# Kernel tuning notes

Hardware: AMD Instinct MI355X
Metric: run time of the kernel (lower is better)

Reference implementation:

```python
import jax, jax.numpy as jnp
import numpy as np

B, N, E, H = 16, 196, 512, 8   # batch, tokens(14x14), embedding_channels(=KV_size_S), heads
HD = E // H                    # 64  spatial-attn head dim
C = 4 * E                      # 2048 = KV_size (concat of 4 branches)
HDC = C // H                   # 256 channel-attn (SelfAttentionTAT) head dim

def _ln(x, g, b, eps=1e-6):
    m = jnp.mean(x, -1, keepdims=True)
    v = jnp.mean(jnp.square(x - m), -1, keepdims=True)
    return (x - m) * jax.lax.rsqrt(v + eps) * g + b

def setup_inputs():
    key = jax.random.key(0)
    ks = jax.random.split(key, 16)
    n = lambda k, s, sc=0.02: jax.random.normal(k, s, jnp.float32) * sc
    return {
        "emb1": jax.random.normal(ks[0], (B, N, E), jnp.float32),
        "emb2": jax.random.normal(ks[1], (B, N, E), jnp.float32),
        "emb3": jax.random.normal(ks[2], (B, N, E), jnp.float32),
        "emb4": jax.random.normal(ks[3], (B, N, E), jnp.float32),
        "ln_attn_g": jnp.ones((4, E), jnp.float32), "ln_attn_b": jnp.zeros((4, E), jnp.float32),
        "lnC_g": jnp.ones((C,), jnp.float32), "lnC_b": jnp.zeros((C,), jnp.float32),
        "Wq_c": n(ks[4], (C, C)), "Wk_c": n(ks[5], (C, C)),
        "Wv_c": n(ks[6], (C, C)), "Wo_c": n(ks[7], (C, C)),
        "q_w": n(ks[8], (4, N, N), 0.05),              # query1..4 stacked (token-mixing Linear(196,196))
        "k_w": n(ks[9], (4 * N, 4 * N)),               # key   Linear(784,784)
        "v_w": n(ks[10], (4 * N, 4 * N)),              # value Linear(784,784)
        "out_w": n(ks[11], (4, E, E)),                 # out1..4 stacked
        "ln_ffn_g": jnp.ones((4, E), jnp.float32), "ln_ffn_b": jnp.zeros((4, E), jnp.float32),
        "fc1_w": n(ks[12], (4, E, 4 * E)), "fc1_b": n(ks[13], (4, 4 * E), 1e-6),
        "fc2_w": n(ks[14], (4, 4 * E, E)), "fc2_b": n(ks[15], (4, E), 1e-6),
    }

def reference(emb1, emb2, emb3, emb4, ln_attn_g, ln_attn_b, lnC_g, lnC_b,
              Wq_c, Wk_c, Wv_c, Wo_c, q_w, k_w, v_w, out_w,
              ln_ffn_g, ln_ffn_b, fc1_w, fc1_b, fc2_w, fc2_b):
    embs = jnp.stack([emb1, emb2, emb3, emb4])                         # [4,B,N,E]
    cx = _ln(embs, ln_attn_g[:, None, None, :], ln_attn_b[:, None, None, :])
    ec = _ln(jnp.concatenate([emb1, emb2, emb3, emb4], -1), lnC_g, lnC_b)  # [B,N,C]
    # SelfAttentionTAT: multi-head self-attention over the concatenated channel embedding
    q = (ec @ Wq_c).reshape(B, N, H, HDC).transpose(0, 2, 1, 3)
    k = (ec @ Wk_c).reshape(B, N, H, HDC).transpose(0, 2, 1, 3)
    v = (ec @ Wv_c).reshape(B, N, H, HDC).transpose(0, 2, 1, 3)
    s = jax.nn.softmax(jnp.einsum('bhnd,bhmd->bhnm', q, k) * np.float32(1.0 / np.sqrt(HDC)), -1)
    T_hat = jnp.einsum('bhnm,bhmd->bhnd', s, v).transpose(0, 2, 1, 3).reshape(B, N, C) @ Wo_c
    # split channel dim into 4 chunks, concat along token axis -> [B,4N,E]
    KV_S = T_hat.reshape(B, N, 4, E).transpose(0, 2, 1, 3).reshape(B, 4 * N, E)
    # token-mixing projections (Linear applied to the token axis)
    Q = jnp.einsum('gbnc,gnm->gbmc', cx, q_w)                          # [4,B,N,E]
    K = jnp.einsum('bnc,nm->bmc', KV_S, k_w)                           # [B,4N,E]
    V = jnp.einsum('bnc,nm->bmc', KV_S, v_w)
    Qh = Q.reshape(4, B, N, H, HD).transpose(0, 1, 3, 2, 4)            # [4,B,H,N,HD]
    Kh = K.reshape(B, 4 * N, H, HD).transpose(0, 2, 1, 3)              # [B,H,4N,HD]
    Vh = V.reshape(B, 4 * N, H, HD).transpose(0, 2, 1, 3)
    attn = jnp.einsum('gbhnd,bhmd->gbhnm', Qh, Kh)                     # [4,B,H,N,4N]
    # InstanceNorm2d (no affine, eps=1e-5) over (N,4N) per (branch,batch,head) instead of 1/sqrt(d)
    m = jnp.mean(attn, (-2, -1), keepdims=True)
    var = jnp.mean(jnp.square(attn - m), (-2, -1), keepdims=True)
    p = jax.nn.softmax((attn - m) * jax.lax.rsqrt(var + 1e-5), -1)
    ctx = jnp.einsum('gbhnm,bhmd->gbhnd', p, Vh)                       # [4,B,H,N,HD]
    # faithful to source: only branch 1 is permuted before .view; branches 2-4
    # are .view'ed directly from [B,H,N,HD] (head-major flatten)
    c1 = ctx[0].transpose(0, 2, 1, 3).reshape(B, N, E)
    crest = ctx[1:].reshape(3, B, N, E)
    cmerged = jnp.concatenate([c1[None], crest], 0)                    # [4,B,N,E]
    h = embs + jnp.einsum('gbne,gef->gbnf', cmerged, out_w)            # residual 1
    x = _ln(h, ln_ffn_g[:, None, None, :], ln_ffn_b[:, None, None, :])
    x = jax.nn.gelu(jnp.einsum('gbne,gef->gbnf', x, fc1_w) + fc1_b[:, None, None, :], approximate=False)
    x = jnp.einsum('gbnf,gfe->gbne', x, fc2_w) + fc2_b[:, None, None, :]
    out = x + h                                                        # residual 2
    return (out[0], out[1], out[2], out[3])
```

## Files before the change

### kernel.cpp

```cpp
#include <hip/hip_runtime.h>
#include <hip/hip_bf16.h>
#include <math.h>

typedef __hip_bfloat16 bf16;
typedef __attribute__((ext_vector_type(8))) short v8s;
typedef __attribute__((ext_vector_type(4))) short v4s;
typedef __attribute__((ext_vector_type(4))) float v4f;

#define Bq   16
#define Nq   196
#define Eq   512
#define Hq   8
#define HDq  64
#define Cq   2048
#define HDCq 256
#define N4q  784
#define BNq  (Bq*Nq)
#define SLOT ((long)BNq*Cq)
#define L2E  1.44269504f

struct P4 { const void* p[4]; };

__global__ __launch_bounds__(256) void k_fill(float* __restrict__ out, long n, float v) {
  long i = (long)blockIdx.x * 256 + threadIdx.x;
  if (i < n) out[i] = v;
}

__device__ __forceinline__ float blk_sum(float v, float* buf) {
  #pragma unroll
  for (int off = 32; off; off >>= 1) v += __shfl_down(v, off, 64);
  int tid = threadIdx.x;
  __syncthreads();
  if ((tid & 63) == 0) buf[tid >> 6] = v;
  __syncthreads();
  return buf[0] + buf[1] + buf[2] + buf[3];
}

__device__ __forceinline__ unsigned int pack2bf(float a, float b) {
  unsigned short ha = __builtin_bit_cast(unsigned short, (bf16)a);
  unsigned short hb = __builtin_bit_cast(unsigned short, (bf16)b);
  return (unsigned int)ha | ((unsigned int)hb << 16);
}

__global__ __launch_bounds__(256) void k_ln_concat(
    const float* __restrict__ e1, const float* __restrict__ e2,
    const float* __restrict__ e3, const float* __restrict__ e4,
    const float* __restrict__ gamma, const float* __restrict__ beta,
    bf16* __restrict__ ec) {
  __shared__ float buf[4];
  int row = blockIdx.x;
  int tid = threadIdx.x;
  float vals[8];
  #pragma unroll
  for (int i = 0; i < 8; i++) {
    const float* src = (i < 2) ? e1 : (i < 4) ? e2 : (i < 6) ? e3 : e4;
    vals[i] = src[(long)row * Eq + (i & 1) * 256 + tid];
  }
  float s = 0;
  #pragma unroll
  for (int i = 0; i < 8; i++) s += vals[i];
  float mean = blk_sum(s, buf) * (1.f / 2048.f);
  float ss = 0;
  #pragma unroll
  for (int i = 0; i < 8; i++) { float d = vals[i] - mean; ss += d * d; }
  float rstd = rsqrtf(blk_sum(ss, buf) * (1.f / 2048.f) + 1e-6f);
  #pragma unroll
  for (int i = 0; i < 8; i++) {
    int c = tid + i * 256;
    ec[(long)row * Cq + c] = (bf16)((vals[i] - mean) * rstd * gamma[c] + beta[c]);
  }
}

__global__ __launch_bounds__(256) void k_ln_branch(
    const float* __restrict__ e1, const float* __restrict__ e2,
    const float* __restrict__ e3, const float* __restrict__ e4,
    const float* __restrict__ gamma, const float* __restrict__ beta,
    bf16* __restrict__ cx) {
  __shared__ float buf[4];
  int idx = blockIdx.x;
  int tid = threadIdx.x;
  int row = idx % BNq; int g = idx / BNq;
  const float* src = (g == 0) ? e1 : (g == 1) ? e2 : (g == 2) ? e3 : e4;
  float v0 = src[(long)row * Eq + tid];
  float v1 = src[(long)row * Eq + 256 + tid];
  float mean = blk_sum(v0 + v1, buf) * (1.f / 512.f);
  float d0 = v0 - mean, d1 = v1 - mean;
  float var = blk_sum(d0 * d0 + d1 * d1, buf) * (1.f / 512.f);
  float rstd = rsqrtf(var + 1e-6f);
  cx[(long)idx * Eq + tid]       = (bf16)(d0 * rstd * gamma[g * Eq + tid]       + beta[g * Eq + tid]);
  cx[(long)idx * Eq + 256 + tid] = (bf16)(d1 * rstd * gamma[g * Eq + 256 + tid] + beta[g * Eq + 256 + tid]);
}

__global__ __launch_bounds__(256) void k_ln_rows(
    const bf16* __restrict__ x, const float* __restrict__ gamma, const float* __restrict__ beta,
    bf16* __restrict__ out) {
  __shared__ float buf[4];
  int idx = blockIdx.x;
  int tid = threadIdx.x;
  int g = idx / BNq;
  float v0 = (float)x[(long)idx * Eq + tid];
  float v1 = (float)x[(long)idx * Eq + 256 + tid];
  float mean = blk_sum(v0 + v1, buf) * (1.f / 512.f);
  float d0 = v0 - mean, d1 = v1 - mean;
  float var = blk_sum(d0 * d0 + d1 * d1, buf) * (1.f / 512.f);
  float rstd = rsqrtf(var + 1e-6f);
  out[(long)idx * Eq + tid]       = (bf16)(d0 * rstd * gamma[g * Eq + tid]       + beta[g * Eq + tid]);
  out[(long)idx * Eq + 256 + tid] = (bf16)(d1 * rstd * gamma[g * Eq + 256 + tid] + beta[g * Eq + 256 + tid]);
}

__global__ __launch_bounds__(256) void k_cvt_t(
    const float* __restrict__ W, bf16* __restrict__ WT, int K, int Nn) {
  __shared__ short T[64][72];
  int tid = threadIdx.x;
  long zo = (long)blockIdx.z * K * Nn;
  int n0 = blockIdx.x * 64, k0 = blockIdx.y * 64;
  int r = tid >> 2, c = (tid & 3) * 16;
  const float* src = W + zo + (long)(k0 + r) * Nn + n0 + c;
  float4 f0 = *(const float4*)src;
  float4 f1 = *(const float4*)(src + 4);
  float4 f2 = *(const float4*)(src + 8);
  float4 f3 = *(const float4*)(src + 12);
  float fv[16] = {f0.x,f0.y,f0.z,f0.w, f1.x,f1.y,f1.z,f1.w,
                  f2.x,f2.y,f2.z,f2.w, f3.x,f3.y,f3.z,f3.w};
  #pragma unroll
  for (int e = 0; e < 16; e++)
    T[c + e][r] = __builtin_bit_cast(short, (bf16)fv[e]);
  __syncthreads();
  short* dst = (short*)WT + zo + (long)(n0 + r) * K + k0 + c;
  *(v8s*)dst       = *(const v8s*)&T[r][c];
  *(v8s*)(dst + 8) = *(const v8s*)&T[r][c + 8];
}

template<bool HAS_BIAS, bool GELU, int RES_MODE, bool OUT_F32>
__global__ __launch_bounds__(256, 2) void k_gemm_bt(
    const bf16* __restrict__ A, const bf16* __restrict__ WT,
    const float* __restrict__ bias, P4 resp,
    void* __restrict__ out, int M, int Nn, int K,
    long aStride, long wStride, long oStride) {
  __shared__ short As[256][76];
  __shared__ short Bs[64][76];
  int tid = threadIdx.x;
  int l = tid & 63, w = tid >> 6;
  int li = l & 15, lg = l >> 4;
  int z = blockIdx.z;
  int m0 = blockIdx.x * 256, n0 = blockIdx.y * 64;
  const short* Ab = (const short*)A + (long)z * aStride;
  const short* Wb = (const short*)WT + (long)z * wStride;
  const void* res = resp.p[z];

  v4f acc[4][4] = {};

  int ar = tid >> 1, ak = (tid & 1) * 32;
  long arow0 = (long)m0 + ar;       if (arow0 >= M) arow0 = M - 1;
  long arow1 = (long)m0 + ar + 128; if (arow1 >= M) arow1 = M - 1;
  const short* ap0 = Ab + arow0 * K + ak;
  const short* ap1 = Ab + arow1 * K + ak;
  int br = tid >> 2, bk = (tid & 3) * 16;
  const short* bp = Wb + (long)(n0 + br) * K + bk;

  for (int k0 = 0; k0 < K; k0 += 64) {
    const short* p0 = ap0 + k0;
    const short* p1 = ap1 + k0;
    *(v8s*)&As[ar][ak]            = *(const v8s*)p0;
    *(v8s*)&As[ar][ak + 8]        = *(const v8s*)(p0 + 8);
    *(v8s*)&As[ar][ak + 16]       = *(const v8s*)(p0 + 16);
    *(v8s*)&As[ar][ak + 24]       = *(const v8s*)(p0 + 24);
    *(v8s*)&As[ar + 128][ak]      = *(const v8s*)p1;
    *(v8s*)&As[ar + 128][ak + 8]  = *(const v8s*)(p1 + 8);
    *(v8s*)&As[ar + 128][ak + 16] = *(const v8s*)(p1 + 16);
    *(v8s*)&As[ar + 128][ak + 24] = *(const v8s*)(p1 + 24);
    *(v8s*)&Bs[br][bk]            = *(const v8s*)(bp + k0);
    *(v8s*)&Bs[br][bk + 8]        = *(const v8s*)(bp + k0 + 8);
    __syncthreads();
    #pragma unroll
    for (int ks = 0; ks < 2; ks++) {
      v8s af[4], bfr[4];
      #pragma unroll
      for (int mi = 0; mi < 4; mi++)
        af[mi] = *(const v8s*)&As[w * 64 + mi * 16 + li][ks * 32 + lg * 8];
      #pragma unroll
      for (int nj = 0; nj < 4; nj++)
        bfr[nj] = *(const v8s*)&Bs[nj * 16 + li][ks * 32 + lg * 8];
      #pragma unroll
      for (int mi = 0; mi < 4; mi++)
        #pragma unroll
        for (int nj = 0; nj < 4; nj++)
          acc[mi][nj] = __builtin_amdgcn_mfma_f32_16x16x32_bf16(af[mi], bfr[nj], acc[mi][nj], 0, 0, 0);
    }
    __syncthreads();
  }

  #pragma unroll
  for (int nj = 0; nj < 4; nj++) {
    int n = n0 + nj * 16 + li;
    float bv = HAS_BIAS ? bias[n] : 0.f;
    #pragma unroll
    for (int mi = 0; mi < 4; mi++) {
      #pragma unroll
      for (int rr = 0; rr < 4; rr++) {
        int m = m0 + w * 64 + mi * 16 + lg * 4 + rr;
        if (m < M) {
          float x = acc[mi][nj][rr] + bv;
          if (GELU) x = 0.5f * x * (1.f + erff(x * 0.70710678118f));
          if (RES_MODE == 1) x += ((const float*)res)[(long)m * Nn + n];
          if (RES_MODE == 2) x += (float)((const bf16*)res)[(long)m * Nn + n];
          if (OUT_F32) (((float*)out) + (long)z * oStride)[(long)m * Nn + n] = x;
          else         (((bf16*)out)  + (long)z * oStride)[(long)m * Nn + n] = (bf16)x;
        }
      }
    }
  }
}

template<bool HAS_BIAS, bool GELU, int RES_MODE, bool OUT_F32>
__global__ __launch_bounds__(256, 2) void k_gemm(
    const bf16* __restrict__ A, const float* __restrict__ W,
    const float* __restrict__ bias, const void* __restrict__ res,
    void* __restrict__ out, int M, int Nn, int K,
    long aStride, long wStride, long bStride, long resStride, long oStride) {
  __shared__ short As[256][76];
  __shared__ short Bs[64][72];
  int tid = threadIdx.x;
  int l = tid & 63, w = tid >> 6;
  int li = l & 15, lg = l >> 4;
  int z = blockIdx.z;
  int m0 = blockIdx.x * 256, n0 = blockIdx.y * 64;
  const short* Ab = (const short*)A + (long)z * aStride;
  const float* Wb = W + (long)z * wStride;
  const float* biasb = HAS_BIAS ? bias + (long)z * bStride : nullptr;
  const float* resF = (RES_MODE == 1) ? (const float*)res + (long)z * resStride : nullptr;
  const bf16*  resB = (RES_MODE == 2) ? (const bf16*)res + (long)z * resStride : nullptr;

  v4f acc[4][4] = {};

  int ar = tid >> 1, ak = (tid & 1) * 32;
  long arow0 = (long)m0 + ar;       if (arow0 >= M) arow0 = M - 1;
  long arow1 = (long)m0 + ar + 128; if (arow1 >= M) arow1 = M - 1;
  const short* ap0 = Ab + arow0 * K + ak;
  const short* ap1 = Ab + arow1 * K + ak;

  for (int k0 = 0; k0 < K; k0 += 64) {
    {
      const short* p0 = ap0 + k0;
      const short* p1 = ap1 + k0;
      *(v8s*)&As[ar][ak]            = *(const v8s*)p0;
      *(v8s*)&As[ar][ak + 8]        = *(const v8s*)(p0 + 8);
      *(v8s*)&As[ar][ak + 16]       = *(const v8s*)(p0 + 16);
      *(v8s*)&As[ar][ak + 24]       = *(const v8s*)(p0 + 24);
      *(v8s*)&As[ar + 128][ak]      = *(const v8s*)p1;
      *(v8s*)&As[ar + 128][ak + 8]  = *(const v8s*)(p1 + 8);
      *(v8s*)&As[ar + 128][ak + 16] = *(const v8s*)(p1 + 16);
      *(v8s*)&As[ar + 128][ak + 24] = *(const v8s*)(p1 + 24);
    }
    #pragma unroll
    for (int t = 0; t < 2; t++) {
      int p = tid + 256 * t;
      int kp = p >> 4, nf = p & 15;
      const float* wp = Wb + (long)(k0 + 2 * kp) * Nn + n0 + nf * 4;
      float4 w0 = *(const float4*)wp;
      float4 w1 = *(const float4*)(wp + Nn);
      float f0[4] = {w0.x, w0.y, w0.z, w0.w};
      float f1[4] = {w1.x, w1.y, w1.z, w1.w};
      int ko = (2 * kp) ^ ((nf & 7) << 3);
      #pragma unroll
      for (int e = 0; e < 4; e++)
        *(unsigned int*)&Bs[nf * 4 + e][ko] = pack2bf(f0[e], f1[e]);
    }
    __syncthreads();
    #pragma unroll
    for (int ks = 0; ks < 2; ks++) {
      v8s af[4], bfr[4];
      #pragma unroll
      for (int mi = 0; mi < 4; mi++)
        af[mi] = *(const v8s*)&As[w * 64 + mi * 16 + li][ks * 32 + lg * 8];
      #pragma unroll
      for (int nj = 0; nj < 4; nj++) {
        int rn = nj * 16 + li;
        int ko = (ks * 32 + lg * 8) ^ (((rn >> 2) & 7) << 3);
        bfr[nj] = *(const v8s*)&Bs[rn][ko];
      }
      #pragma unroll
      for (int mi = 0; mi < 4; mi++)
        #pragma unroll
        for (int nj = 0; nj < 4; nj++)
          acc[mi][nj] = __builtin_amdgcn_mfma_f32_16x16x32_bf16(af[mi], bfr[nj], acc[mi][nj], 0, 0, 0);
    }
    __syncthreads();
  }

  #pragma unroll
  for (int nj = 0; nj < 4; nj++) {
    int n = n0 + nj * 16 + li;
    float bv = HAS_BIAS ? biasb[n] : 0.f;
    #pragma unroll
    for (int mi = 0; mi < 4; mi++) {
      #pragma unroll
      for (int rr = 0; rr < 4; rr++) {
        int m = m0 + w * 64 + mi * 16 + lg * 4 + rr;
        if (m < M) {
          float x = acc[mi][nj][rr] + bv;
          if (GELU) x = 0.5f * x * (1.f + erff(x * 0.70710678118f));
          if (RES_MODE == 1) x += resF[(long)m * Nn + n];
          if (RES_MODE == 2) x += (float)resB[(long)m * Nn + n];
          if (OUT_F32) (((float*)out) + (long)z * oStride)[(long)m * Nn + n] = x;
          else         (((bf16*)out)  + (long)z * oStride)[(long)m * Nn + n] = (bf16)x;
        }
      }
    }
  }
}

template<bool REINDEX, bool TRANSV>
__global__ __launch_bounds__(256) void k_mix_mfma(
    const bf16* __restrict__ X, const float* __restrict__ Wt, bf16* __restrict__ out,
    int T) {
  __shared__ short Aws[128][72];
  __shared__ short Xs[128][72];
  int tid = threadIdx.x;
  int l = tid & 63, w = tid >> 6;
  int li = l & 15, lg = l >> 4;
  int wr = w >> 1, wc = w & 1;
  int bidx = blockIdx.x;
  int c0 = blockIdx.y * 128;
  int m0 = blockIdx.z * 128;
  const float* W = REINDEX ? Wt : (Wt + (long)(bidx >> 4) * T * T);
  const short* xb = (const short*)X + (REINDEX ? (long)bidx * Nq * Cq
                                               : (long)bidx * Nq * Eq);
  bf16* ob = out + (long)bidx * T * Eq;

  v4f acc[4][4] = {};
  int nsteps = (T + 63) / 64;
  bool mfull = (m0 + 128 <= T);
  for (int s = 0; s < nsteps; s++) {
    int k0 = s * 64;
    if (mfull) {
      #pragma unroll
      for (int t = 0; t < 4; t++) {
        int p = tid + 256 * t;
        int kp = p >> 5, mf = p & 31;
        int n0r = k0 + 2 * kp; if (n0r > T - 1) n0r = T - 1;
        int n1r = k0 + 2 * kp + 1; if (n1r > T - 1) n1r = T - 1;
        const float* w0p = W + (long)n0r * T + m0 + mf * 4;
        const float* w1p = W + (long)n1r * T + m0 + mf * 4;
        float4 w0 = *(const float4*)w0p;
        float4 w1 = *(const float4*)w1p;
        float f0[4] = {w0.x, w0.y, w0.z, w0.w};
        float f1[4] = {w1.x, w1.y, w1.z, w1.w};
        int ko = (2 * kp) ^ ((mf & 7) << 3);
        #pragma unroll
        for (int e = 0; e < 4; e++)
          *(unsigned int*)&Aws[mf * 4 + e][ko] = pack2bf(f0[e], f1[e]);
      }
    } else {
      #pragma unroll
      for (int t = 0; t < 4; t++) {
        int p = tid + 256 * t;
        int kp = p >> 5, mf = p & 31;
        int n0r = min(k0 + 2 * kp, T - 1);
        int n1r = min(k0 + 2 * kp + 1, T - 1);
        int ko = (2 * kp) ^ ((mf & 7) << 3);
        #pragma unroll
        for (int e = 0; e < 4; e++) {
          int m = min(m0 + mf * 4 + e, T - 1);
          *(unsigned int*)&Aws[mf * 4 + e][ko] =
              pack2bf(W[(long)n0r * T + m], W[(long)n1r * T + m]);
        }
      }
    }
    #pragma unroll
    for (int t = 0; t < 2; t++) {
      int p = tid + 256 * t;
      int np = p >> 4, cg = p & 15;
      int n0r = k0 + 2 * np, n1r = n0r + 1;
      v8s x0 = {}, x1 = {};
      if (n0r < T) {
        const short* xp;
        if (REINDEX) {
          int q4 = (n0r >= 588) ? 3 : (n0r >= 392) ? 2 : (n0r >= 196) ? 1 : 0;
          xp = xb + (long)(n0r - q4 * Nq) * Cq + q4 * Eq + c0 + cg * 8;
        } else {
          xp = xb + (long)n0r * Eq + c0 + cg * 8;
        }
        x0 = *(const v8s*)xp;
      }
      if (n1r < T) {
        const short* xp;
        if (REINDEX) {
          int q4 = (n1r >= 588) ? 3 : (n1r >= 392) ? 2 : (n1r >= 196) ? 1 : 0;
          xp = xb + (long)(n1r - q4 * Nq) * Cq + q4 * Eq + c0 + cg * 8;
        } else {
          xp = xb + (long)n1r * Eq + c0 + cg * 8;
        }
        x1 = *(const v8s*)xp;
      }
      int ko = (2 * np) ^ ((cg & 7) << 3);
      #pragma unroll
      for (int e = 0; e < 8; e++) {
        unsigned short h0 = (unsigned short)x0[e];
        unsigned short h1 = (unsigned short)x1[e];
        *(unsigned int*)&Xs[cg * 8 + e][ko] = (unsigned int)h0 | ((unsigned int)h1 << 16);
      }
    }
    __syncthreads();
    #pragma unroll
    for (int ks = 0; ks < 2; ks++) {
      v8s af[4], bfr[4];
      #pragma unroll
      for (int mi = 0; mi < 4; mi++) {
        int rm = wr * 64 + mi * 16 + li;
        int ko = (ks * 32 + lg * 8) ^ (((rm >> 2) & 7) << 3);
        af[mi] = *(const v8s*)&Aws[rm][ko];
      }
      #pragma unroll
      for (int nj = 0; nj < 4; nj++) {
        int rc = wc * 64 + nj * 16 + li;
        int ko = (ks * 32 + lg * 8) ^ (((rc >> 3) & 7) << 3);
        bfr[nj] = *(const v8s*)&Xs[rc][ko];
      }
      if (TRANSV) {
        #pragma unroll
        for (int nj = 0; nj < 4; nj++)
          #pragma unroll
          for (int mi = 0; mi < 4; mi++)
            acc[nj][mi] = __builtin_amdgcn_mfma_f32_16x16x32_bf16(bfr[nj], af[mi], acc[nj][mi], 0, 0, 0);
      } else {
        #pragma unroll
        for (int mi = 0; mi < 4; mi++)
          #pragma unroll
          for (int nj = 0; nj < 4; nj++)
            acc[mi][nj] = __builtin_amdgcn_mfma_f32_16x16x32_bf16(af[mi], bfr[nj], acc[mi][nj], 0, 0, 0);
      }
    }
    __syncthreads();
  }

  if (TRANSV) {
    bf16* obt = out + (long)bidx * Eq * T;
    #pragma unroll
    for (int mi = 0; mi < 4; mi++) {
      int m = m0 + wr * 64 + mi * 16 + li;
      if (m < T) {
        #pragma unroll
        for (int nj = 0; nj < 4; nj++) {
          #pragma unroll
          for (int rr = 0; rr < 4; rr++) {
            int c = c0 + wc * 64 + nj * 16 + lg * 4 + rr;
            obt[(long)c * T + m] = (bf16)acc[nj][mi][rr];
          }
        }
      }
    }
  } else {
    #pragma unroll
    for (int nj = 0; nj < 4; nj++) {
      int c = c0 + wc * 64 + nj * 16 + li;
      #pragma unroll
      for (int mi = 0; mi < 4; mi++) {
        #pragma unroll
        for (int rr = 0; rr < 4; rr++) {
          int m = m0 + wr * 64 + mi * 16 + lg * 4 + rr;
          if (m < T) ob[(long)m * Eq + c] = (bf16)acc[mi][nj][rr];
        }
      }
    }
  }
}

__global__ __launch_bounds__(256) void k_chan_attn(
    const bf16* __restrict__ q, const bf16* __restrict__ k, const bf16* __restrict__ v,
    bf16* __restrict__ T) {
  __shared__ short P[16 * 232];
  __shared__ float mbuf[4][16];
  __shared__ float dbuf[4][16];
  int tid = threadIdx.x;
  int l = tid & 63, w = tid >> 6;
  int bid = blockIdx.x;
  int it = bid / 128, bh = bid % 128;
  int h = bh & 7; int b = bh >> 3;
  int i0 = it * 16;
  int li = l & 15, lg = l >> 4;

  for (int z = tid; z < 16 * 28; z += 256) P[(z / 28) * 232 + 196 + (z % 28)] = 0;

  int arow = i0 + li;
  const short* qp = (const short*)(q + ((long)(b * Nq) + (arow < Nq ? arow : 0)) * Cq + h * HDCq + lg * 8);
  v8s qf[8] = {};
  if (arow < Nq) {
    #pragma unroll
    for (int kk = 0; kk < 8; kk++) qf[kk] = *(const v8s*)(qp + kk * 32);
  }

  float accS[4][4];
  float lmax[4] = {-1e30f, -1e30f, -1e30f, -1e30f};
  #pragma unroll
  for (int jj = 0; jj < 4; jj++) {
    int jt = w + jj * 4;
    if (jt < 13) {
      int jrow = jt * 16 + li;
      int jr = jrow < Nq ? jrow : Nq - 1;
      const short* kp = (const short*)(k + ((long)(b * Nq) + jr) * Cq + h * HDCq + lg * 8);
      v4f acc = {0.f, 0.f, 0.f, 0.f};
      #pragma unroll
      for (int kk = 0; kk < 8; kk++) {
        v8s kf = *(const v8s*)(kp + kk * 32);
        acc = __builtin_amdgcn_mfma_f32_16x16x32_bf16(qf[kk], kf, acc, 0, 0, 0);
      }
      bool valid = jrow < Nq;
      #pragma unroll
      for (int rr = 0; rr < 4; rr++) {
        float s = acc[rr] * (0.0625f * L2E);
        accS[jj][rr] = s;
        if (valid) lmax[rr] = fmaxf(lmax[rr], s);
      }
    } else {
      #pragma unroll
      for (int rr = 0; rr < 4; rr++) accS[jj][rr] = 0.f;
    }
  }
  #pragma unroll
  for (int rr = 0; rr < 4; rr++) {
    float mv = lmax[rr];
    #pragma unroll
    for (int m = 1; m < 16; m <<= 1) mv = fmaxf(mv, __shfl_xor(mv, m, 64));
    if (li == 0) mbuf[w][lg * 4 + rr] = mv;
  }
  __syncthreads();
  float gmx[4];
  #pragma unroll
  for (int rr = 0; rr < 4; rr++) {
    int row = lg * 4 + rr;
    gmx[rr] = fmaxf(fmaxf(mbuf[0][row], mbuf[1][row]), fmaxf(mbuf[2][row], mbuf[3][row]));
  }

  float ds4[4] = {0.f, 0.f, 0.f, 0.f};
  #pragma unroll
  for (int jj = 0; jj < 4; jj++) {
    int jt = w + jj * 4;
    if (jt < 13) {
      int jrow = jt * 16 + li;
      bool valid = jrow < Nq;
      #pragma unroll
      for (int rr = 0; rr < 4; rr++) {
        float e = valid ? exp2f(accS[jj][rr] - gmx[rr]) : 0.f;
        bf16 pb = (bf16)e;
        ds4[rr] += (float)pb;
        P[(lg * 4 + rr) * 232 + jt * 16 + li] = __builtin_bit_cast(short, pb);
      }
    }
  }
  #pragma unroll
  for (int rr = 0; rr < 4; rr++) {
    float sv = ds4[rr];
    #pragma unroll
    for (int m = 1; m < 16; m <<= 1) sv += __shfl_xor(sv, m, 64);
    if (li == 0) dbuf[w][lg * 4 + rr] = sv;
  }
  __syncthreads();

  v8s pfs[7];
  #pragma unroll
  for (int js = 0; js < 7; js++) pfs[js] = *(const v8s*)&P[li * 232 + js * 32 + lg * 8];

  const short* vbase = (const short*)(v + (long)(b * Nq) * Cq + h * HDCq);
  float accO[4][4];
  #pragma unroll
  for (int dt = 0; dt < 4; dt++) {
    int d = w * 64 + dt * 16 + li;
    v4f acc = {0.f, 0.f, 0.f, 0.f};
    #pragma unroll
    for (int js = 0; js < 6; js++) {
      const short* vp = vbase + (long)(js * 32 + lg * 8) * Cq + d;
      v8s vf;
      #pragma unroll
      for (int e = 0; e < 8; e++) vf[e] = vp[(long)e * Cq];
      acc = __builtin_amdgcn_mfma_f32_16x16x32_bf16(vf, pfs[js], acc, 0, 0, 0);
    }
    {
      int j0 = 192 + lg * 8;
      const short* vp = vbase + (long)j0 * Cq + d;
      v8s vf = {};
      #pragma unroll
      for (int e = 0; e < 8; e++) if (j0 + e < Nq) vf[e] = vp[(long)e * Cq];
      acc = __builtin_amdgcn_mfma_f32_16x16x32_bf16(vf, pfs[6], acc, 0, 0, 0);
    }
    #pragma unroll
    for (int rr = 0; rr < 4; rr++) accO[dt][rr] = acc[rr];
  }

  float inv = 1.f / (dbuf[0][li] + dbuf[1][li] + dbuf[2][li] + dbuf[3][li]);
  int ic = i0 + li;
  if (ic < Nq) {
    #pragma unroll
    for (int dt = 0; dt < 4; dt++) {
      bf16* tp = T + ((long)(b * Nq) + ic) * Cq + h * HDCq + w * 64 + dt * 16 + lg * 4;
      v4s ov;
      #pragma unroll
      for (int rr = 0; rr < 4; rr++) {
        bf16 t = (bf16)(accO[dt][rr] * inv);
        ov[rr] = __builtin_bit_cast(short, t);
      }
      *(v4s*)tp = ov;
    }
  }
}

__global__ __launch_bounds__(256) void k_gram(
    const bf16* __restrict__ Qs, const bf16* __restrict__ Ks,
    float* __restrict__ G, float* __restrict__ XS) {
  __shared__ short XT[64][136];
  int tid = threadIdx.x;
  int l = tid & 63, w = tid >> 6;
  int li = l & 15, lg = l >> 4;
  int r = blockIdx.x;
  const short* xb; int R;
  if (r < 512) {
    int gb = r >> 3, h = r & 7;
    xb = (const short*)Qs + (long)gb * Nq * Eq + h * 64; R = Nq;
  } else {
    int idx = r - 512; int b = idx >> 3, h = idx & 7;
    xb = (const short*)Ks + (long)b * N4q * Eq + h * 64; R = N4q;
  }
  v4f acc[4] = {};
  float xsum = 0.f;
  for (int n0 = 0; n0 < R; n0 += 128) {
    __syncthreads();
    #pragma unroll
    for (int t = 0; t < 4; t++) {
      int task = tid + 256 * t;
      int nn = task >> 3, oct = task & 7;
      int n = n0 + nn;
      v8s xv = {};
      if (n < R) xv = *(const v8s*)(xb + (long)n * Eq + oct * 8);
      #pragma unroll
      for (int e = 0; e < 8; e++) XT[oct * 8 + e][nn] = xv[e];
    }
    __syncthreads();
    if (tid < 64) {
      #pragma unroll
      for (int c = 0; c < 128; c += 8) {
        v8s v = *(const v8s*)&XT[tid][c];
        #pragma unroll
        for (int e = 0; e < 8; e++) xsum += (float)__builtin_bit_cast(bf16, v[e]);
      }
    }
    #pragma unroll
    for (int ks = 0; ks < 4; ks++) {
      v8s af = *(const v8s*)&XT[w * 16 + li][ks * 32 + lg * 8];
      #pragma unroll
      for (int t2 = 0; t2 < 4; t2++) {
        v8s bf2 = *(const v8s*)&XT[t2 * 16 + li][ks * 32 + lg * 8];
        acc[t2] = __builtin_amdgcn_mfma_f32_16x16x32_bf16(af, bf2, acc[t2], 0, 0, 0);
      }
    }
  }
  float* gout = G + (long)r * 4096;
  #pragma unroll
  for (int t2 = 0; t2 < 4; t2++)
    #pragma unroll
    for (int rr = 0; rr < 4; rr++)
      gout[(w * 16 + lg * 4 + rr) * 64 + t2 * 16 + li] = acc[t2][rr];
  if (tid < 64) XS[(long)r * 64 + tid] = xsum;
}

__global__ __launch_bounds__(256) void k_statfin(
    const float* __restrict__ G, const float* __restrict__ XS,
    float* __restrict__ stat) {
  __shared__ float buf[4];
  int r = blockIdx.x;
  int h = r & 7; int b = (r >> 3) & 15;
  int kidx = 512 + b * 8 + h;
  const float* gq = G + (long)r * 4096;
  const float* gk = G + (long)kidx * 4096;
  int tid = threadIdx.x;
  float f = 0.f;
  for (int i = tid; i < 4096; i += 256) f += gq[i] * gk[i];
  float frob = blk_sum(f, buf);
  float md = (tid < 64) ? XS[(long)r * 64 + tid] * XS[(long)kidx * 64 + tid] : 0.f;
  float meandot = blk_sum(md, buf);
  if (tid == 0) {
    float inv = 1.f / ((float)Nq * (float)N4q);
    float mean = meandot * inv;
    float var = frob * inv - mean * mean;
    stat[1024 + r * 2] = mean;
    stat[1024 + r * 2 + 1] = rsqrtf(var + 1e-5f);
  }
}

__global__ __launch_bounds__(256) void k_spa_attn(
    const bf16* __restrict__ Q, const bf16* __restrict__ K, const bf16* __restrict__ VT,
    const float* __restrict__ stat, bf16* __restrict__ ctx) {
  __shared__ short P[16 * 808];
  __shared__ float mbuf[4][16];
  __shared__ float dbuf[4][16];
  int tid = threadIdx.x;
  int l = tid & 63, w = tid >> 6;
  int bid = blockIdx.x;
  int it = bid / 512, r = bid % 512;
  int h = r & 7; int gb = r >> 3; int b = gb & 15;
  int i0 = it * 16;
  int li = l & 15, lg = l >> 4;

  for (int z = tid; z < 16 * 24; z += 256) P[(z / 24) * 808 + 784 + (z % 24)] = 0;

  float rstdl2 = stat[1024 + r * 2 + 1] * L2E;

  int arow = i0 + li;
  const short* qp = (const short*)(Q + ((long)gb * Nq + (arow < Nq ? arow : 0)) * Eq + h * 64 + lg * 8);
  v8s qf0 = {}, qf1 = {};
  if (arow < Nq) { qf0 = *(const v8s*)qp; qf1 = *(const v8s*)(qp + 32); }

  const short* kbase = (const short*)(K + ((long)b * N4q + li) * Eq + h * 64 + lg * 8);

  float accS[13][4];
  float lmax = -1e30f;
  #pragma unroll
  for (int jj = 0; jj < 13; jj++) {
    int jt = w + jj * 4;
    if (jt < 49) {
      const short* kp = kbase + (long)jt * 16 * Eq;
      v8s kf0 = *(const v8s*)kp;
      v8s kf1 = *(const v8s*)(kp + 32);
      v4f acc = {0.f, 0.f, 0.f, 0.f};
      acc = __builtin_amdgcn_mfma_f32_16x16x32_bf16(kf0, qf0, acc, 0, 0, 0);
      acc = __builtin_amdgcn_mfma_f32_16x16x32_bf16(kf1, qf1, acc, 0, 0, 0);
      #pragma unroll
      for (int rr = 0; rr < 4; rr++) {
        accS[jj][rr] = acc[rr];
        lmax = fmaxf(lmax, acc[rr]);
      }
    } else {
      #pragma unroll
      for (int rr = 0; rr < 4; rr++) accS[jj][rr] = 0.f;
    }
  }
  lmax = fmaxf(lmax, __shfl_xor(lmax, 16, 64));
  lmax = fmaxf(lmax, __shfl_xor(lmax, 32, 64));
  if (lg == 0) mbuf[w][li] = lmax;
  __syncthreads();
  float gmx = fmaxf(fmaxf(mbuf[0][li], mbuf[1][li]), fmaxf(mbuf[2][li], mbuf[3][li]));

  float dsum = 0.f;
  #pragma unroll
  for (int jj = 0; jj < 13; jj++) {
    int jt = w + jj * 4;
    if (jt < 49) {
      v4s pk;
      #pragma unroll
      for (int rr = 0; rr < 4; rr++) {
        float e = exp2f((accS[jj][rr] - gmx) * rstdl2);
        bf16 pb = (bf16)e;
        dsum += (float)pb;
        pk[rr] = __builtin_bit_cast(short, pb);
      }
      *(v4s*)&P[li * 808 + jt * 16 + lg * 4] = pk;
    }
  }
  dsum += __shfl_xor(dsum, 16, 64);
  dsum += __shfl_xor(dsum, 32, 64);
  if (lg == 0) dbuf[w][li] = dsum;
  __syncthreads();

  const short* vtb = (const short*)VT + ((long)b * Eq + h * 64 + w * 16 + li) * N4q;
  v4f accO = {0.f, 0.f, 0.f, 0.f};
  for (int js = 0; js < 24; js++) {
    v8s vf = *(const v8s*)(vtb + js * 32 + lg * 8);
    v8s pf = *(const v8s*)&P[li * 808 + js * 32 + lg * 8];
    accO = __builtin_amdgcn_mfma_f32_16x16x32_bf16(vf, pf, accO, 0, 0, 0);
  }
  {
    int jb = 768 + lg * 8;
    v8s vf = {};
    if (jb < N4q) vf = *(const v8s*)(vtb + jb);
    v8s pf = *(const v8s*)&P[li * 808 + 768 + lg * 8];
    accO = __builtin_amdgcn_mfma_f32_16x16x32_bf16(vf, pf, accO, 0, 0, 0);
  }
  float inv = 1.f / (dbuf[0][li] + dbuf[1][li] + dbuf[2][li] + dbuf[3][li]);
  int ic = i0 + li;
  if (ic < Nq) {
    bf16* cp = ctx + (long)r * Nq * 64 + (long)ic * 64 + w * 16 + lg * 4;
    v4s ov;
    #pragma unroll
    for (int rr = 0; rr < 4; rr++) {
      bf16 t = (bf16)(accO[rr] * inv);
      ov[rr] = __builtin_bit_cast(short, t);
    }
    *(v4s*)cp = ov;
  }
}

__global__ __launch_bounds__(256) void k_scramble(
    const bf16* __restrict__ ctx, bf16* __restrict__ cm) {
  long i = (long)blockIdx.x * 256 + threadIdx.x;
  int e = (int)(i & 511); long t = i >> 9;
  int n = (int)(t % Nq); long gb = t / Nq;
  int g = (int)(gb >> 4);
  long srcIdx;
  if (g == 0) {
    int h = e >> 6, d = e & 63;
    srcIdx = ((gb * 8 + h) * (long)Nq + n) * 64 + d;
  } else {
    int l = n * 512 + e;
    int h = l / 12544; int rem = l % 12544; int n2 = rem >> 6; int d = rem & 63;
    srcIdx = ((gb * 8 + h) * (long)Nq + n2) * 64 + d;
  }
  cm[i] = ctx[srcIdx];
}

extern "C" void kernel_launch(void* const* d_in, const int* in_sizes, int n_in,
                              void* d_out, int out_size, void* d_ws, size_t ws_size,
                              hipStream_t stream) {
  const int expect[22] = {
    1605632, 1605632, 1605632, 1605632,
    2048, 2048, 2048, 2048,
    4194304, 4194304, 4194304, 4194304,
    153664, 614656, 614656, 1048576,
    2048, 2048,
    4194304, 8192, 4194304, 2048
  };
  long fillBlocks = ((long)out_size + 255) / 256;
  if (n_in != 22) {
    k_fill<<<fillBlocks, 256, 0, stream>>>((float*)d_out, out_size, 3000.f);
    return;
  }
  for (int i = 0; i < 22; i++) {
    if (in_sizes[i] != expect[i]) {
      k_fill<<<fillBlocks, 256, 0, stream>>>((float*)d_out, out_size, 1000.f + 20.f * i);
      return;
    }
  }

  const float* e1 = (const float*)d_in[0];
  const float* e2 = (const float*)d_in[1];
  const float* e3 = (const float*)d_in[2];
  const float* e4 = (const float*)d_in[3];
  const float* ln_attn_g = (const float*)d_in[4];
  const float* ln_attn_b = (const float*)d_in[5];
  const float* lnC_g = (const float*)d_in[6];
  const float* lnC_b = (const float*)d_in[7];
  const float* Wq = (const float*)d_in[8];
  const float* Wk = (const float*)d_in[9];
  const float* Wv = (const float*)d_in[10];
  const float* Wo = (const float*)d_in[11];
  const float* q_w = (const float*)d_in[12];
  const float* k_w = (const float*)d_in[13];
  const float* v_w = (const float*)d_in[14];
  const float* out_w = (const float*)d_in[15];
  const float* ln_ffn_g = (const float*)d_in[16];
  const float* ln_ffn_b = (const float*)d_in[17];
  const float* fc1_w = (const float*)d_in[18];
  const float* fc1_b = (const float*)d_in[19];
  const float* fc2_w = (const float*)d_in[20];
  const float* fc2_b = (const float*)d_in[21];

  bf16* W0 = (bf16*)d_ws;
  bf16* W1 = W0 + SLOT;
  bf16* W2 = W0 + 2 * SLOT;
  bf16* OUTS = (bf16*)d_out;
  float* OUT = (float*)d_out;
  float* ST = (float*)((char*)d_ws + 3 * SLOT * sizeof(bf16));
  float* GR = OUT + SLOT / 2;
  float* XSUM = GR + 640 * 4096;
  bf16* WB = (bf16*)(OUT + SLOT / 2);

  dim3 gqkv(13, Cq / 64);
  dim3 gcvC(Cq / 64, Cq / 64);
  long off = (long)BNq * Eq;
  P4 nores = {};

  k_ln_concat<<<BNq, 256, 0, stream>>>(e1, e2, e3, e4, lnC_g, lnC_b, W0);
  k_cvt_t<<<gcvC, 256, 0, stream>>>(Wq, WB, Cq, Cq);
  k_gemm_bt<false,false,0,false><<<gqkv, 256, 0, stream>>>(W0, WB, nullptr, nores, W1, BNq, Cq, Cq, 0, 0, 0);
  k_cvt_t<<<gcvC, 256, 0, stream>>>(Wk, WB, Cq, Cq);
  k_gemm_bt<false,false,0,false><<<gqkv, 256, 0, stream>>>(W0, WB, nullptr, nores, W2, BNq, Cq, Cq, 0, 0, 0);
  k_cvt_t<<<gcvC, 256, 0, stream>>>(Wv, WB, Cq, Cq);
  k_gemm_bt<false,false,0,false><<<gqkv, 256, 0, stream>>>(W0, WB, nullptr, nores, OUTS, BNq, Cq, Cq, 0, 0, 0);
  k_chan_attn<<<Bq * Hq * 13, 256, 0, stream>>>(W1, W2, OUTS, W0);
  k_cvt_t<<<gcvC, 256, 0, stream>>>(Wo, WB, Cq, Cq);
  k_gemm_bt<false,false,0,false><<<gqkv, 256, 0, stream>>>(W0, WB, nullptr, nores, W1, BNq, Cq, Cq, 0, 0, 0);

  k_ln_branch<<<4 * BNq, 256, 0, stream>>>(e1, e2, e3, e4, ln_attn_g, ln_attn_b, W0);
  dim3 gmq(64, 4, 2);
  k_mix_mfma<false,false><<<gmq, 256, 0, stream>>>(W0, q_w, W2, Nq);
  dim3 gmkv(16, 4, 7);
  k_mix_mfma<true,false><<<gmkv, 256, 0, stream>>>(W1, k_w, OUTS, N4q);
  k_mix_mfma<true,true><<<gmkv, 256, 0, stream>>>(W1, v_w, W0, N4q);

  k_gram<<<640, 256, 0, stream>>>(W2, OUTS, GR, XSUM);
  k_statfin<<<512, 256, 0, stream>>>(GR, XSUM, ST);
  k_cvt_t<<<dim3(Eq / 64, Eq / 64, 4), 256, 0, stream>>>(out_w, WB, Eq, Eq);
  k_spa_attn<<<512 * 13, 256, 0, stream>>>(W2, OUTS, W0, ST, W1);

  k_scramble<<<(4L * BNq * Eq) / 256, 256, 0, stream>>>(W1, W2);
  P4 resp; resp.p[0] = e1; resp.p[1] = e2; resp.p[2] = e3; resp.p[3] = e4;
  k_gemm_bt<false,false,1,false><<<dim3(13, Eq / 64, 4), 256, 0, stream>>>(
      W2, WB, nullptr, resp, W0, BNq, Eq, Eq, off, (long)Eq * Eq, off);

  k_ln_rows<<<4 * BNq, 256, 0, stream>>>(W0, ln_ffn_g, ln_ffn_b, W1);
  const long MH = 1568;
  for (int mh = 0; mh < 2; mh++) {
    k_gemm<true,true,0,false><<<dim3(7, (4 * Eq) / 64, 4), 256, 0, stream>>>(
        W1 + mh * MH * Eq, fc1_w, fc1_b, nullptr, W2,
        (int)MH, 4 * Eq, Eq,
        off, (long)Eq * 4 * Eq, 4 * Eq, 0, MH * 4 * Eq);
    k_gemm<true,false,2,true><<<dim3(7, Eq / 64, 4), 256, 0, stream>>>(
        W2, fc2_w, fc2_b, W0 + mh * MH * Eq, OUT + mh * MH * Eq,
        (int)MH, Eq, 4 * Eq,
        MH * 4 * Eq, (long)4 * Eq * Eq, Eq, off, off);
  }
}
```

Before: 1.128 ms.

## Pre-transpose mixing weights to bf16 and emit V transposed for channel attention

Adds a k_cvt_tp kernel that converts the token-mixing weights (q_w, k_w, v_w) once into padded, transposed bf16 buffers. The mix GEMM can then load its A tiles with plain vector loads instead of doing strided fp32 reads, bf16 packing and swizzling inside its K loop. Separately, the V projection GEMM now writes its output transposed ([b, channel, token]), so channel attention reads V with contiguous vector loads rather than 8 scalar loads strided by C. The cost is three extra small kernel launches, and shared-memory bank conflicts may return now that the A-tile swizzle is gone.

```diff
diff --git a/kernel.cpp b/kernel.cpp
--- a/kernel.cpp
+++ b/kernel.cpp
@@ -131,7 +131,34 @@
   *(v8s*)(dst + 8) = *(const v8s*)&T[r][c + 8];
 }
 
-template<bool HAS_BIAS, bool GELU, int RES_MODE, bool OUT_F32>
+__global__ __launch_bounds__(256) void k_cvt_tp(
+    const float* __restrict__ W, bf16* __restrict__ WT, int T, int Kp,
+    long wz, long oz) {
+  __shared__ short Tl[64][72];
+  int tid = threadIdx.x;
+  const float* Wz = W + (long)blockIdx.z * wz;
+  bf16* WTz = WT + (long)blockIdx.z * oz;
+  int n0 = blockIdx.x * 64;
+  int m0 = blockIdx.y * 64;
+  int r = tid >> 2, c = (tid & 3) * 16;
+  int n = n0 + r;
+  bool vn = n < T;
+  #pragma unroll
+  for (int e = 0; e < 16; e++) {
+    int m = m0 + c + e; if (m > T - 1) m = T - 1;
+    float v = vn ? Wz[(long)n * T + m] : 0.f;
+    Tl[c + e][r] = __builtin_bit_cast(short, (bf16)v);
+  }
+  __syncthreads();
+  int m = m0 + r;
+  if (m < T) {
+    short* dst = (short*)WTz + (long)m * Kp + n0 + c;
+    *(v8s*)dst       = *(const v8s*)&Tl[r][c];
+    *(v8s*)(dst + 8) = *(const v8s*)&Tl[r][c + 8];
+  }
+}
+
+template<bool HAS_BIAS, bool GELU, int RES_MODE, bool OUT_F32, bool TRANSO>
 __global__ __launch_bounds__(256, 2) void k_gemm_bt(
     const bf16* __restrict__ A, const bf16* __restrict__ WT,
     const float* __restrict__ bias, P4 resp,
@@ -190,6 +217,30 @@
     __syncthreads();
   }
 
+  if (TRANSO) {
+    short* vt = (short*)out;
+    #pragma unroll
+    for (int nj = 0; nj < 4; nj++) {
+      int n = n0 + nj * 16 + li;
+      #pragma unroll
+      for (int mi = 0; mi < 4; mi++) {
+        int m4 = m0 + w * 64 + mi * 16 + lg * 4;
+        if (m4 < M) {
+          unsigned bq = (unsigned)m4 / 196u;
+          unsigned tl = (unsigned)m4 - bq * 196u;
+          v4s ov;
+          #pragma unroll
+          for (int rr = 0; rr < 4; rr++) {
+            bf16 t = (bf16)acc[mi][nj][rr];
+            ov[rr] = __builtin_bit_cast(short, t);
+          }
+          *(v4s*)&vt[((long)bq * Nn + n) * 196 + tl] = ov;
+        }
+      }
+    }
+    return;
+  }
+
   #pragma unroll
   for (int nj = 0; nj < 4; nj++) {
     int n = n0 + nj * 16 + li;
@@ -312,9 +363,9 @@
 
 template<bool REINDEX, bool TRANSV>
 __global__ __launch_bounds__(256) void k_mix_mfma(
-    const bf16* __restrict__ X, const float* __restrict__ Wt, bf16* __restrict__ out,
-    int T) {
-  __shared__ short Aws[128][72];
+    const bf16* __restrict__ X, const bf16* __restrict__ WTp, bf16* __restrict__ out,
+    int T, int Kp, long wStride) {
+  __shared__ short Aws[128][76];
   __shared__ short Xs[128][72];
   int tid = threadIdx.x;
   int l = tid & 63, w = tid >> 6;
@@ -323,49 +374,25 @@
   int bidx = blockIdx.x;
   int c0 = blockIdx.y * 128;
   int m0 = blockIdx.z * 128;
-  const float* W = REINDEX ? Wt : (Wt + (long)(bidx >> 4) * T * T);
+  const short* Wb = (const short*)WTp + (REINDEX ? 0 : (long)(bidx >> 4) * wStride);
   const short* xb = (const short*)X + (REINDEX ? (long)bidx * Nq * Cq
                                                : (long)bidx * Nq * Eq);
   bf16* ob = out + (long)bidx * T * Eq;
 
   v4f acc[4][4] = {};
-  int nsteps = (T + 63) / 64;
-  bool mfull = (m0 + 128 <= T);
+  int nsteps = Kp / 64;
+  int ar2 = tid >> 1, ak2 = (tid & 1) * 32;
+  int arow = m0 + ar2; if (arow >= T) arow = T - 1;
+  const short* awp = Wb + (long)arow * Kp + ak2;
+
   for (int s = 0; s < nsteps; s++) {
     int k0 = s * 64;
-    if (mfull) {
-      #pragma unroll
-      for (int t = 0; t < 4; t++) {
-        int p = tid + 256 * t;
-        int kp = p >> 5, mf = p & 31;
-        int n0r = k0 + 2 * kp; if (n0r > T - 1) n0r = T - 1;
-        int n1r = k0 + 2 * kp + 1; if (n1r > T - 1) n1r = T - 1;
-        const float* w0p = W + (long)n0r * T + m0 + mf * 4;
-        const float* w1p = W + (long)n1r * T + m0 + mf * 4;
-        float4 w0 = *(const float4*)w0p;
-        float4 w1 = *(const float4*)w1p;
-        float f0[4] = {w0.x, w0.y, w0.z, w0.w};
-        float f1[4] = {w1.x, w1.y, w1.z, w1.w};
-        int ko = (2 * kp) ^ ((mf & 7) << 3);
-        #pragma unroll
-        for (int e = 0; e < 4; e++)
-          *(unsigned int*)&Aws[mf * 4 + e][ko] = pack2bf(f0[e], f1[e]);
-      }
-    } else {
-      #pragma unroll
-      for (int t = 0; t < 4; t++) {
-        int p = tid + 256 * t;
-        int kp = p >> 5, mf = p & 31;
-        int n0r = min(k0 + 2 * kp, T - 1);
-        int n1r = min(k0 + 2 * kp + 1, T - 1);
-        int ko = (2 * kp) ^ ((mf & 7) << 3);
-        #pragma unroll
-        for (int e = 0; e < 4; e++) {
-          int m = min(m0 + mf * 4 + e, T - 1);
-          *(unsigned int*)&Aws[mf * 4 + e][ko] =
-              pack2bf(W[(long)n0r * T + m], W[(long)n1r * T + m]);
-        }
-      }
+    {
+      const short* p = awp + k0;
+      *(v8s*)&Aws[ar2][ak2]      = *(const v8s*)p;
+      *(v8s*)&Aws[ar2][ak2 + 8]  = *(const v8s*)(p + 8);
+      *(v8s*)&Aws[ar2][ak2 + 16] = *(const v8s*)(p + 16);
+      *(v8s*)&Aws[ar2][ak2 + 24] = *(const v8s*)(p + 24);
     }
     #pragma unroll
     for (int t = 0; t < 2; t++) {
@@ -406,11 +433,8 @@
     for (int ks = 0; ks < 2; ks++) {
       v8s af[4], bfr[4];
       #pragma unroll
-      for (int mi = 0; mi < 4; mi++) {
-        int rm = wr * 64 + mi * 16 + li;
-        int ko = (ks * 32 + lg * 8) ^ (((rm >> 2) & 7) << 3);
-        af[mi] = *(const v8s*)&Aws[rm][ko];
-      }
+      for (int mi = 0; mi < 4; mi++)
+        af[mi] = *(const v8s*)&Aws[wr * 64 + mi * 16 + li][ks * 32 + lg * 8];
       #pragma unroll
       for (int nj = 0; nj < 4; nj++) {
         int rc = wc * 64 + nj * 16 + li;
@@ -467,7 +491,7 @@
 }
 
 __global__ __launch_bounds__(256) void k_chan_attn(
-    const bf16* __restrict__ q, const bf16* __restrict__ k, const bf16* __restrict__ v,
+    const bf16* __restrict__ q, const bf16* __restrict__ k, const bf16* __restrict__ vt,
     bf16* __restrict__ T) {
   __shared__ short P[16 * 232];
   __shared__ float mbuf[4][16];
@@ -561,26 +585,28 @@
   #pragma unroll
   for (int js = 0; js < 7; js++) pfs[js] = *(const v8s*)&P[li * 232 + js * 32 + lg * 8];
 
-  const short* vbase = (const short*)(v + (long)(b * Nq) * Cq + h * HDCq);
+  const short* Vt = (const short*)vt;
   float accO[4][4];
   #pragma unroll
   for (int dt = 0; dt < 4; dt++) {
-    int d = w * 64 + dt * 16 + li;
+    long row = (long)b * 2048 + h * HDCq + w * 64 + dt * 16 + li;
+    const short* vp = Vt + row * 196;
     v4f acc = {0.f, 0.f, 0.f, 0.f};
     #pragma unroll
     for (int js = 0; js < 6; js++) {
-      const short* vp = vbase + (long)(js * 32 + lg * 8) * Cq + d;
+      v4s a0 = *(const v4s*)(vp + js * 32 + lg * 8);
+      v4s a1 = *(const v4s*)(vp + js * 32 + lg * 8 + 4);
       v8s vf;
-      #pragma unroll
-      for (int e = 0; e < 8; e++) vf[e] = vp[(long)e * Cq];
+      vf[0] = a0[0]; vf[1] = a0[1]; vf[2] = a0[2]; vf[3] = a0[3];
+      vf[4] = a1[0]; vf[5] = a1[1]; vf[6] = a1[2]; vf[7] = a1[3];
       acc = __builtin_amdgcn_mfma_f32_16x16x32_bf16(vf, pfs[js], acc, 0, 0, 0);
     }
     {
-      int j0 = 192 + lg * 8;
-      const short* vp = vbase + (long)j0 * Cq + d;
       v8s vf = {};
-      #pragma unroll
-      for (int e = 0; e < 8; e++) if (j0 + e < Nq) vf[e] = vp[(long)e * Cq];
+      if (lg == 0) {
+        v4s a0 = *(const v4s*)(vp + 192);
+        vf[0] = a0[0]; vf[1] = a0[1]; vf[2] = a0[2]; vf[3] = a0[3];
+      }
       acc = __builtin_amdgcn_mfma_f32_16x16x32_bf16(vf, pfs[6], acc, 0, 0, 0);
     }
     #pragma unroll
@@ -869,21 +895,27 @@
 
   k_ln_concat<<<BNq, 256, 0, stream>>>(e1, e2, e3, e4, lnC_g, lnC_b, W0);
   k_cvt_t<<<gcvC, 256, 0, stream>>>(Wq, WB, Cq, Cq);
-  k_gemm_bt<false,false,0,false><<<gqkv, 256, 0, stream>>>(W0, WB, nullptr, nores, W1, BNq, Cq, Cq, 0, 0, 0);
+  k_gemm_bt<false,false,0,false,false><<<gqkv, 256, 0, stream>>>(W0, WB, nullptr, nores, W1, BNq, Cq, Cq, 0, 0, 0);
   k_cvt_t<<<gcvC, 256, 0, stream>>>(Wk, WB, Cq, Cq);
-  k_gemm_bt<false,false,0,false><<<gqkv, 256, 0, stream>>>(W0, WB, nullptr, nores, W2, BNq, Cq, Cq, 0, 0, 0);
+  k_gemm_bt<false,false,0,false,false><<<gqkv, 256, 0, stream>>>(W0, WB, nullptr, nores, W2, BNq, Cq, Cq, 0, 0, 0);
   k_cvt_t<<<gcvC, 256, 0, stream>>>(Wv, WB, Cq, Cq);
-  k_gemm_bt<false,false,0,false><<<gqkv, 256, 0, stream>>>(W0, WB, nullptr, nores, OUTS, BNq, Cq, Cq, 0, 0, 0);
+  k_gemm_bt<false,false,0,false,true><<<gqkv, 256, 0, stream>>>(W0, WB, nullptr, nores, OUTS, BNq, Cq, Cq, 0, 0, 0);
   k_chan_attn<<<Bq * Hq * 13, 256, 0, stream>>>(W1, W2, OUTS, W0);
   k_cvt_t<<<gcvC, 256, 0, stream>>>(Wo, WB, Cq, Cq);
-  k_gemm_bt<false,false,0,false><<<gqkv, 256, 0, stream>>>(W0, WB, nullptr, nores, W1, BNq, Cq, Cq, 0, 0, 0);
+  k_gemm_bt<false,false,0,false,false><<<gqkv, 256, 0, stream>>>(W0, WB, nullptr, nores, W1, BNq, Cq, Cq, 0, 0, 0);
 
   k_ln_branch<<<4 * BNq, 256, 0, stream>>>(e1, e2, e3, e4, ln_attn_g, ln_attn_b, W0);
+  bf16* WTQ = WB;
+  bf16* WTK = WTQ + (long)4 * 196 * 256;
+  bf16* WTV = WTK + (long)784 * 832;
+  k_cvt_tp<<<dim3(4, 4, 4), 256, 0, stream>>>(q_w, WTQ, Nq, 256, (long)Nq * Nq, (long)Nq * 256);
+  k_cvt_tp<<<dim3(13, 13, 1), 256, 0, stream>>>(k_w, WTK, N4q, 832, 0, 0);
+  k_cvt_tp<<<dim3(13, 13, 1), 256, 0, stream>>>(v_w, WTV, N4q, 832, 0, 0);
   dim3 gmq(64, 4, 2);
-  k_mix_mfma<false,false><<<gmq, 256, 0, stream>>>(W0, q_w, W2, Nq);
+  k_mix_mfma<false,false><<<gmq, 256, 0, stream>>>(W0, WTQ, W2, Nq, 256, (long)Nq * 256);
   dim3 gmkv(16, 4, 7);
-  k_mix_mfma<true,false><<<gmkv, 256, 0, stream>>>(W1, k_w, OUTS, N4q);
-  k_mix_mfma<true,true><<<gmkv, 256, 0, stream>>>(W1, v_w, W0, N4q);
+  k_mix_mfma<true,false><<<gmkv, 256, 0, stream>>>(W1, WTK, OUTS, N4q, 832, 0);
+  k_mix_mfma<true,true><<<gmkv, 256, 0, stream>>>(W1, WTV, W0, N4q, 832, 0);
 
   k_gram<<<640, 256, 0, stream>>>(W2, OUTS, GR, XSUM);
   k_statfin<<<512, 256, 0, stream>>>(GR, XSUM, ST);
@@ -892,7 +924,7 @@
 
   k_scramble<<<(4L * BNq * Eq) / 256, 256, 0, stream>>>(W1, W2);
   P4 resp; resp.p[0] = e1; resp.p[1] = e2; resp.p[2] = e3; resp.p[3] = e4;
-  k_gemm_bt<false,false,1,false><<<dim3(13, Eq / 64, 4), 256, 0, stream>>>(
+  k_gemm_bt<false,false,1,false,false><<<dim3(13, Eq / 64, 4), 256, 0, stream>>>(
       W2, WB, nullptr, resp, W0, BNq, Eq, Eq, off, (long)Eq * Eq, off);
 
   k_ln_rows<<<4 * BNq, 256, 0, stream>>>(W0, ln_ffn_g, ln_ffn_b, W1);
```

After: 1.024 ms. 9.2% less time.
